# Performance work log

Measured on AMD Instinct MI355X. Metric: run time of the kernel, lower is better.

## Reference

```python
import jax, jax.numpy as jnp
import numpy as np

N_EDGES = 1_600_000
D_FEAT = 32
N_NODES = 50_000


def setup_inputs() -> dict:
    key = jax.random.key(0)
    k1, k2, k3, k4 = jax.random.split(key, 4)
    m = jax.random.normal(k1, (N_EDGES, D_FEAT), dtype=jnp.float32)
    dst = jax.random.randint(k2, (N_EDGES,), 0, N_NODES, dtype=jnp.int64)
    w = jax.random.normal(k3, (4,), dtype=jnp.float32)
    b = jax.random.normal(k4, (1,), dtype=jnp.float32)
    return {"m": m, "dst": dst, "w": w, "b": b, "n_nodes": N_NODES}


def reference(m, dst, w, b, n_nodes):
    # Four segment reductions edge->node over destination index (copy_e_*)
    s = jax.ops.segment_sum(m, dst, num_segments=n_nodes)            # [N, D]
    mn = jax.ops.segment_min(m, dst, num_segments=n_nodes)
    mx = jax.ops.segment_max(m, dst, num_segments=n_nodes)
    deg = jax.ops.segment_sum(jnp.ones((m.shape[0],), m.dtype), dst,
                              num_segments=n_nodes)                  # [N]
    has = (deg > 0)[:, None]
    # DGL returns 0 for zero-degree nodes
    mn = jnp.where(has, mn, 0.0)
    mx = jnp.where(has, mx, 0.0)
    mean = s / jnp.maximum(deg, 1.0)[:, None]
    stacked = jnp.stack([s, mn, mx, mean], axis=-1)                  # [N, D, 4]
    out = jnp.einsum('ndk,k->nd', stacked, w) + b[0]                 # Dense(4,1) + squeeze
    return out
```

## Files before the change

### kernel.cpp

```cpp
#include <hip/hip_runtime.h>
#include <math.h>

#define D_FEAT 32
#define BSHIFT 6
#define NODES_PER_BKT 64
#define TILE 8192
#define PT 32
#define MAXBKT 1024
#define CAP 4096

__global__ void hist_kernel(const int* __restrict__ dst, int* __restrict__ bucketCount,
                            int E, int nbucket) {
    __shared__ int h[MAXBKT];
    for (int i = threadIdx.x; i < nbucket; i += 256) h[i] = 0;
    __syncthreads();
    int tbase = blockIdx.x * TILE;
    #pragma unroll 4
    for (int k = 0; k < PT; k++) {
        int e = tbase + k * 256 + threadIdx.x;
        if (e < E) atomicAdd(&h[dst[e] >> BSHIFT], 1);
    }
    __syncthreads();
    for (int i = threadIdx.x; i < nbucket; i += 256) {
        int c = h[i];
        if (c) atomicAdd(&bucketCount[i], c);
    }
}

__global__ void scan_kernel(const int* __restrict__ bucketCount,
                            int* __restrict__ bucketBase, int* __restrict__ bucketCursor,
                            int nbucket, int E) {
    __shared__ int lds[256];
    int tid = threadIdx.x;
    int vals[4];
    int s = 0;
    #pragma unroll
    for (int k = 0; k < 4; k++) {
        int i = tid * 4 + k;
        vals[k] = (i < nbucket) ? bucketCount[i] : 0;
        s += vals[k];
    }
    lds[tid] = s;
    __syncthreads();
    for (int off = 1; off < 256; off <<= 1) {
        int t = (tid >= off) ? lds[tid - off] : 0;
        __syncthreads();
        lds[tid] += t;
        __syncthreads();
    }
    int run = lds[tid] - s;
    #pragma unroll
    for (int k = 0; k < 4; k++) {
        int i = tid * 4 + k;
        if (i < nbucket) { bucketBase[i] = run; bucketCursor[i] = run; }
        run += vals[k];
    }
    if (tid == 0) bucketBase[nbucket] = E;
}

__global__ void partition_kernel(const int* __restrict__ dst,
                                 int* __restrict__ bucketCursor,
                                 unsigned int* __restrict__ keys,
                                 int E, int nbucket) {
    __shared__ int h[MAXBKT];
    __shared__ int baseL[MAXBKT];
    int tid = threadIdx.x;
    for (int i = tid; i < nbucket; i += 256) h[i] = 0;
    __syncthreads();
    int tbase = blockIdx.x * TILE;
    int pk[PT];
    #pragma unroll 4
    for (int k = 0; k < PT; k++) {
        int e = tbase + k * 256 + tid;
        if (e < E) {
            int b = dst[e] >> BSHIFT;
            int r = atomicAdd(&h[b], 1);
            pk[k] = (b << 13) | r;
        } else pk[k] = -1;
    }
    __syncthreads();
    for (int i = tid; i < nbucket; i += 256) {
        int c = h[i];
        baseL[i] = c ? atomicAdd(&bucketCursor[i], c) : 0;
    }
    __syncthreads();
    #pragma unroll 4
    for (int k = 0; k < PT; k++) {
        if (pk[k] >= 0) {
            int e = tbase + k * 256 + tid;
            int d = dst[e];
            int b = pk[k] >> 13;
            int r = pk[k] & 8191;
            keys[baseL[b] + r] = ((unsigned)(d & (NODES_PER_BKT - 1)) << 26) | (unsigned)e;
        }
    }
}

__global__ void bucket_gather_kernel(const float* __restrict__ m,
                                     const unsigned int* __restrict__ keys,
                                     const int* __restrict__ bucketBase,
                                     const float* __restrict__ w,
                                     const float* __restrict__ bia,
                                     float* __restrict__ out, int N) {
    __shared__ int nh[NODES_PER_BKT];
    __shared__ int noff[NODES_PER_BKT + 1];
    __shared__ int ncur[NODES_PER_BKT];
    __shared__ int seid[CAP];
    int bkt = blockIdx.x;
    int tid = threadIdx.x;
    int start = bucketBase[bkt];
    int cnt = bucketBase[bkt + 1] - start;
    if (cnt > CAP) cnt = CAP;

    if (tid < NODES_PER_BKT) nh[tid] = 0;
    __syncthreads();
    for (int i = tid; i < cnt; i += 256)
        atomicAdd(&nh[keys[start + i] >> 26], 1);
    __syncthreads();
    if (tid < NODES_PER_BKT) {
        int v = nh[tid];
        int x = v;
        #pragma unroll
        for (int off = 1; off < 64; off <<= 1) {
            int t = __shfl_up(x, off, 64);
            if (tid >= off) x += t;
        }
        noff[tid + 1] = x;
        if (tid == 0) noff[0] = 0;
        ncur[tid] = x - v;
    }
    __syncthreads();
    for (int i = tid; i < cnt; i += 256) {
        unsigned int k = keys[start + i];
        int pos = atomicAdd(&ncur[k >> 26], 1);
        seid[pos] = (int)(k & 0x03FFFFFFu);
    }
    __syncthreads();

    int hw = tid >> 5;
    int f  = tid & 31;
    int nodeBase = bkt << BSHIFT;
    float w0 = w[0], w1 = w[1], w2 = w[2], w3 = w[3], bb = bia[0];
    for (int nl = hw; nl < NODES_PER_BKT; nl += 8) {
        int node = nodeBase + nl;
        if (node >= N) break;
        int s0 = noff[nl], e0 = noff[nl + 1];
        int deg = e0 - s0;
        float s = 0.0f, mn = INFINITY, mx = -INFINITY;
        int j = s0;
        for (; j + 4 <= e0; j += 4) {
            int e0i = seid[j], e1i = seid[j + 1], e2i = seid[j + 2], e3i = seid[j + 3];
            float v0 = m[e0i * D_FEAT + f];
            float v1 = m[e1i * D_FEAT + f];
            float v2 = m[e2i * D_FEAT + f];
            float v3 = m[e3i * D_FEAT + f];
            s += v0; mn = fminf(mn, v0); mx = fmaxf(mx, v0);
            s += v1; mn = fminf(mn, v1); mx = fmaxf(mx, v1);
            s += v2; mn = fminf(mn, v2); mx = fmaxf(mx, v2);
            s += v3; mn = fminf(mn, v3); mx = fmaxf(mx, v3);
        }
        for (; j < e0; j++) {
            float v = m[seid[j] * D_FEAT + f];
            s += v; mn = fminf(mn, v); mx = fmaxf(mx, v);
        }
        bool has = deg > 0;
        float mean = s / fmaxf((float)deg, 1.0f);
        out[node * D_FEAT + f] = w0 * s + w1 * (has ? mn : 0.0f)
                               + w2 * (has ? mx : 0.0f) + w3 * mean + bb;
    }
}

extern "C" void kernel_launch(void* const* d_in, const int* in_sizes, int n_in,
                              void* d_out, int out_size, void* d_ws, size_t ws_size,
                              hipStream_t stream) {
    const float* m   = (const float*)d_in[0];
    const int*   dst = (const int*)  d_in[1];
    const float* w   = (const float*)d_in[2];
    const float* b   = (const float*)d_in[3];

    int E = in_sizes[0] / D_FEAT;
    int N = out_size    / D_FEAT;
    int nbucket = (N + NODES_PER_BKT - 1) >> BSHIFT;

    int* ws           = (int*)d_ws;
    int* bucketCount  = ws;
    int* bucketBase   = bucketCount + MAXBKT;
    int* bucketCursor = bucketBase + MAXBKT + 1;
    unsigned int* keys = (unsigned int*)(bucketCursor + MAXBKT);

    int nTiles = (E + TILE - 1) / TILE;

    hipMemsetAsync(bucketCount, 0, MAXBKT * sizeof(int), stream);
    hipLaunchKernelGGL(hist_kernel, dim3(nTiles), dim3(256), 0, stream,
                       dst, bucketCount, E, nbucket);
    hipLaunchKernelGGL(scan_kernel, dim3(1), dim3(256), 0, stream,
                       bucketCount, bucketBase, bucketCursor, nbucket, E);
    hipLaunchKernelGGL(partition_kernel, dim3(nTiles), dim3(256), 0, stream,
                       dst, bucketCursor, keys, E, nbucket);
    hipLaunchKernelGGL(bucket_gather_kernel, dim3(nbucket), dim3(256), 0, stream,
                       m, keys, bucketBase, w, b, (float*)d_out, N);
}
```

Baseline: 357.7 us.

## Vectorize dst loads, cache bucket keys in LDS, deepen gather unroll

The histogram and partition kernels now read dst as int4, four indices per load. Partition packs each edge's local node id into its register key so dst is not read a second time. The gather kernel stages each bucket's keys in shared memory rather than reading them from global memory twice, and unrolls the edge loop to 8 for more outstanding loads. This drops the E%4 tail, so it assumes E is divisible by 4. The extra 16KB of shared memory may reduce occupancy in the gather kernel.

```diff
diff --git a/kernel.cpp b/kernel.cpp
--- a/kernel.cpp
+++ b/kernel.cpp
@@ -10,15 +10,22 @@
 #define CAP 4096
 
 __global__ void hist_kernel(const int* __restrict__ dst, int* __restrict__ bucketCount,
-                            int E, int nbucket) {
+                            int E4, int nbucket) {
     __shared__ int h[MAXBKT];
     for (int i = threadIdx.x; i < nbucket; i += 256) h[i] = 0;
     __syncthreads();
-    int tbase = blockIdx.x * TILE;
-    #pragma unroll 4
-    for (int k = 0; k < PT; k++) {
-        int e = tbase + k * 256 + threadIdx.x;
-        if (e < E) atomicAdd(&h[dst[e] >> BSHIFT], 1);
+    const int4* dst4 = (const int4*)dst;
+    int tbase4 = blockIdx.x * (TILE / 4);
+    #pragma unroll
+    for (int k = 0; k < PT / 4; k++) {
+        int i4 = tbase4 + k * 256 + threadIdx.x;
+        if (i4 < E4) {
+            int4 d = dst4[i4];
+            atomicAdd(&h[d.x >> BSHIFT], 1);
+            atomicAdd(&h[d.y >> BSHIFT], 1);
+            atomicAdd(&h[d.z >> BSHIFT], 1);
+            atomicAdd(&h[d.w >> BSHIFT], 1);
+        }
     }
     __syncthreads();
     for (int i = threadIdx.x; i < nbucket; i += 256) {
@@ -61,22 +68,32 @@
 __global__ void partition_kernel(const int* __restrict__ dst,
                                  int* __restrict__ bucketCursor,
                                  unsigned int* __restrict__ keys,
-                                 int E, int nbucket) {
+                                 int E4, int nbucket) {
     __shared__ int h[MAXBKT];
     __shared__ int baseL[MAXBKT];
     int tid = threadIdx.x;
     for (int i = tid; i < nbucket; i += 256) h[i] = 0;
     __syncthreads();
-    int tbase = blockIdx.x * TILE;
+    const int4* dst4 = (const int4*)dst;
+    int tbase4 = blockIdx.x * (TILE / 4);
     int pk[PT];
-    #pragma unroll 4
-    for (int k = 0; k < PT; k++) {
-        int e = tbase + k * 256 + tid;
-        if (e < E) {
-            int b = dst[e] >> BSHIFT;
-            int r = atomicAdd(&h[b], 1);
-            pk[k] = (b << 13) | r;
-        } else pk[k] = -1;
+    #pragma unroll
+    for (int k = 0; k < PT / 4; k++) {
+        int i4 = tbase4 + k * 256 + tid;
+        if (i4 < E4) {
+            int4 d = dst4[i4];
+            int b0 = d.x >> BSHIFT; int r0 = atomicAdd(&h[b0], 1);
+            int b1 = d.y >> BSHIFT; int r1 = atomicAdd(&h[b1], 1);
+            int b2 = d.z >> BSHIFT; int r2 = atomicAdd(&h[b2], 1);
+            int b3 = d.w >> BSHIFT; int r3 = atomicAdd(&h[b3], 1);
+            pk[4 * k + 0] = (b0 << 19) | ((d.x & 63) << 13) | r0;
+            pk[4 * k + 1] = (b1 << 19) | ((d.y & 63) << 13) | r1;
+            pk[4 * k + 2] = (b2 << 19) | ((d.z & 63) << 13) | r2;
+            pk[4 * k + 3] = (b3 << 19) | ((d.w & 63) << 13) | r3;
+        } else {
+            pk[4 * k + 0] = -1; pk[4 * k + 1] = -1;
+            pk[4 * k + 2] = -1; pk[4 * k + 3] = -1;
+        }
     }
     __syncthreads();
     for (int i = tid; i < nbucket; i += 256) {
@@ -84,28 +101,35 @@
         baseL[i] = c ? atomicAdd(&bucketCursor[i], c) : 0;
     }
     __syncthreads();
-    #pragma unroll 4
-    for (int k = 0; k < PT; k++) {
-        if (pk[k] >= 0) {
-            int e = tbase + k * 256 + tid;
-            int d = dst[e];
-            int b = pk[k] >> 13;
-            int r = pk[k] & 8191;
-            keys[baseL[b] + r] = ((unsigned)(d & (NODES_PER_BKT - 1)) << 26) | (unsigned)e;
-        }
-    }
-}
-
-__global__ void bucket_gather_kernel(const float* __restrict__ m,
-                                     const unsigned int* __restrict__ keys,
-                                     const int* __restrict__ bucketBase,
-                                     const float* __restrict__ w,
-                                     const float* __restrict__ bia,
-                                     float* __restrict__ out, int N) {
+    #pragma unroll
+    for (int k = 0; k < PT / 4; k++) {
+        int i4 = tbase4 + k * 256 + tid;
+        int e = i4 * 4;
+        #pragma unroll
+        for (int l = 0; l < 4; l++) {
+            int p = pk[4 * k + l];
+            if (p >= 0) {
+                int b   = p >> 19;
+                int loc = (p >> 13) & 63;
+                int r   = p & 8191;
+                keys[baseL[b] + r] = ((unsigned)loc << 26) | (unsigned)(e + l);
+            }
+        }
+    }
+}
+
+__global__ __launch_bounds__(256) void bucket_gather_kernel(
+        const float* __restrict__ m,
+        const unsigned int* __restrict__ keys,
+        const int* __restrict__ bucketBase,
+        const float* __restrict__ w,
+        const float* __restrict__ bia,
+        float* __restrict__ out, int N) {
+    __shared__ unsigned int ukey[CAP];
+    __shared__ int seid[CAP];
     __shared__ int nh[NODES_PER_BKT];
     __shared__ int noff[NODES_PER_BKT + 1];
     __shared__ int ncur[NODES_PER_BKT];
-    __shared__ int seid[CAP];
     int bkt = blockIdx.x;
     int tid = threadIdx.x;
     int start = bucketBase[bkt];
@@ -114,8 +138,11 @@
 
     if (tid < NODES_PER_BKT) nh[tid] = 0;
     __syncthreads();
-    for (int i = tid; i < cnt; i += 256)
-        atomicAdd(&nh[keys[start + i] >> 26], 1);
+    for (int i = tid; i < cnt; i += 256) {
+        unsigned int k = keys[start + i];
+        ukey[i] = k;
+        atomicAdd(&nh[k >> 26], 1);
+    }
     __syncthreads();
     if (tid < NODES_PER_BKT) {
         int v = nh[tid];
@@ -131,7 +158,7 @@
     }
     __syncthreads();
     for (int i = tid; i < cnt; i += 256) {
-        unsigned int k = keys[start + i];
+        unsigned int k = ukey[i];
         int pos = atomicAdd(&ncur[k >> 26], 1);
         seid[pos] = (int)(k & 0x03FFFFFFu);
     }
@@ -148,16 +175,23 @@
         int deg = e0 - s0;
         float s = 0.0f, mn = INFINITY, mx = -INFINITY;
         int j = s0;
-        for (; j + 4 <= e0; j += 4) {
-            int e0i = seid[j], e1i = seid[j + 1], e2i = seid[j + 2], e3i = seid[j + 3];
-            float v0 = m[e0i * D_FEAT + f];
-            float v1 = m[e1i * D_FEAT + f];
-            float v2 = m[e2i * D_FEAT + f];
-            float v3 = m[e3i * D_FEAT + f];
+        for (; j + 8 <= e0; j += 8) {
+            float v0 = m[seid[j]     * D_FEAT + f];
+            float v1 = m[seid[j + 1] * D_FEAT + f];
+            float v2 = m[seid[j + 2] * D_FEAT + f];
+            float v3 = m[seid[j + 3] * D_FEAT + f];
+            float v4 = m[seid[j + 4] * D_FEAT + f];
+            float v5 = m[seid[j + 5] * D_FEAT + f];
+            float v6 = m[seid[j + 6] * D_FEAT + f];
+            float v7 = m[seid[j + 7] * D_FEAT + f];
             s += v0; mn = fminf(mn, v0); mx = fmaxf(mx, v0);
             s += v1; mn = fminf(mn, v1); mx = fmaxf(mx, v1);
             s += v2; mn = fminf(mn, v2); mx = fmaxf(mx, v2);
             s += v3; mn = fminf(mn, v3); mx = fmaxf(mx, v3);
+            s += v4; mn = fminf(mn, v4); mx = fmaxf(mx, v4);
+            s += v5; mn = fminf(mn, v5); mx = fmaxf(mx, v5);
+            s += v6; mn = fminf(mn, v6); mx = fmaxf(mx, v6);
+            s += v7; mn = fminf(mn, v7); mx = fmaxf(mx, v7);
         }
         for (; j < e0; j++) {
             float v = m[seid[j] * D_FEAT + f];
@@ -180,6 +214,7 @@
 
     int E = in_sizes[0] / D_FEAT;
     int N = out_size    / D_FEAT;
+    int E4 = E / 4;
     int nbucket = (N + NODES_PER_BKT - 1) >> BSHIFT;
 
     int* ws           = (int*)d_ws;
@@ -192,11 +227,11 @@
 
     hipMemsetAsync(bucketCount, 0, MAXBKT * sizeof(int), stream);
     hipLaunchKernelGGL(hist_kernel, dim3(nTiles), dim3(256), 0, stream,
-                       dst, bucketCount, E, nbucket);
+                       dst, bucketCount, E4, nbucket);
     hipLaunchKernelGGL(scan_kernel, dim3(1), dim3(256), 0, stream,
                        bucketCount, bucketBase, bucketCursor, nbucket, E);
     hipLaunchKernelGGL(partition_kernel, dim3(nTiles), dim3(256), 0, stream,
-                       dst, bucketCursor, keys, E, nbucket);
+                       dst, bucketCursor, keys, E4, nbucket);
     hipLaunchKernelGGL(bucket_gather_kernel, dim3(nbucket), dim3(256), 0, stream,
                        m, keys, bucketBase, w, b, (float*)d_out, N);
 }
```

New measurement: 338.1 us. 1.06x faster.
